# Performance work log

Measured on AMD Instinct MI355X. Metric: run time of the kernel, lower is better.

## Reference

```python
import jax, jax.numpy as jnp
import numpy as np

LAYER_SPECS = [(2, 4, 1), (2, 4, 1), (1, 4, 1), (1, 4, 1)]
SKIPS = [(k - s) * d for (s, k, d) in LAYER_SPECS]  # (ksz-stride)*dilation
C = 80  # encoder channels


def _conv1d(x, w, b, stride, dilation):
    # x: (N, Cin, L), w: (Cout, Cin, K)
    out = jax.lax.conv_general_dilated(
        x, w, window_strides=(stride,), padding='VALID',
        rhs_dilation=(dilation,), dimension_numbers=('NCH', 'OIH', 'NCH'))
    return out + b[None, :, None]


def _encoder(x, w_wide, b_wide, w_1x1, b_1x1, w_f0, b_f0, w_f1, b_f1):
    # x: (N, T, 80) -> (N, T', 80)
    x = jnp.transpose(x, (0, 2, 1))  # (N, 80, T)
    for i, ((stride, ksz, dil), skip) in enumerate(zip(LAYER_SPECS, SKIPS)):
        x1 = _conv1d(x, w_wide[i], b_wide[i], stride, dil)  # (N, 2C, L')
        a, g = jnp.split(x1, 2, axis=1)
        x2 = jnp.tanh(a) * jax.nn.sigmoid(g)                # gated activation
        x3 = _conv1d(x2, w_1x1[i], b_1x1[i], 1, 1)          # (N, C, L')
        if i == 0:
            x = x3
        else:
            T3 = x3.shape[2]
            # residual: strided slice of previous x, take last of each stride group
            res = x[:, :, skip:skip + T3 * stride].reshape(x.shape[0], C, T3, stride)[:, :, :, -1]
            x = x3 + res
    x = _conv1d(jax.nn.relu(_conv1d(x, w_f0, b_f0, 1, 1)), w_f1, b_f1, 1, 1)
    return jnp.transpose(x, (0, 2, 1))  # (N, T', 80)


def setup_inputs() -> dict:
    key = jax.random.key(0)
    ks = jax.random.split(key, 10)
    N, Ts, Tq = 16, 8192, 2048
    return {
        'search': jax.random.normal(ks[0], (N, Ts, 80), dtype=jnp.float32),
        'query': jax.random.normal(ks[1], (N, Tq, 80), dtype=jnp.float32),
        'w_wide': jax.random.normal(ks[2], (4, 160, 80, 4), dtype=jnp.float32) * 0.02,
        'b_wide': jnp.zeros((4, 160), dtype=jnp.float32),
        'w_1x1': jax.random.normal(ks[3], (4, 80, 80, 1), dtype=jnp.float32) * 0.05,
        'b_1x1': jnp.zeros((4, 80), dtype=jnp.float32),
        'w_f0': jax.random.normal(ks[4], (80, 80, 1), dtype=jnp.float32) * 0.05,
        'b_f0': jnp.zeros((80,), dtype=jnp.float32),
        'w_f1': jax.random.normal(ks[5], (80, 80, 1), dtype=jnp.float32) * 0.05,
        'b_f1': jax.random.normal(ks[6], (80,), dtype=jnp.float32) * 0.05,
        'embedding': jax.random.normal(ks[7], (1, 512, 80), dtype=jnp.float32) * 0.001,
        'w_lin': jax.random.normal(ks[8], (2, 80), dtype=jnp.float32) * 0.05,
        'b_lin': jnp.zeros((2,), dtype=jnp.float32),
    }


def reference(search, query, w_wide, b_wide, w_1x1, b_1x1,
              w_f0, b_f0, w_f1, b_f1, embedding, w_lin, b_lin):
    enc_s = _encoder(search, w_wide, b_wide, w_1x1, b_1x1, w_f0, b_f0, w_f1, b_f1)
    enc_q = _encoder(query, w_wide, b_wide, w_1x1, b_1x1, w_f0, b_f0, w_f1, b_f1)

    # ---- VectorQuant (no normalize): nearest-codeword lookup + straight-through ----
    x = enc_s[:, :, None, :]                  # (N, T, 1, V)
    N, T, nc, V = x.shape
    n_classes = embedding.shape[1]
    x1 = x.reshape(N * T, nc, V)              # (NT, 1, V)
    # squared-distance via expansion: argmin identical to argmin of L2 norm
    x2 = jnp.sum(x1 * x1, axis=-1, keepdims=True)          # (NT, 1, 1)
    e2 = jnp.sum(embedding * embedding, axis=-1)[None]     # (1, 1, K)
    xe = jnp.einsum('ncv,ckv->nck', x1, embedding)         # (NT, 1, K)
    idx = jnp.argmin(x2 - 2.0 * xe + e2, axis=2)           # (NT, 1)
    offset = jnp.arange(nc) * n_classes
    flat = embedding.reshape(-1, V)
    output = flat[(idx + offset[None, :]).reshape(-1)].reshape(x.shape)
    out0 = jax.lax.stop_gradient(output - x) + x           # straight-through
    discrete = out0[:, :, 0, :]               # (N, Ts', V)

    # ---- align query to search length, classify, max-pool over time ----
    sf = discrete.shape[1] // enc_q.shape[1]
    q = jnp.tile(enc_q, (1, sf, 1))
    pad = discrete.shape[1] - q.shape[1]
    q = jnp.pad(q, ((0, 0), (0, pad), (0, 0)))
    pred = jnp.tanh((q + discrete) @ w_lin.T + b_lin)      # (N, Ts', 2)
    return jnp.max(pred, axis=1)                           # (N, 2)
```

## Files before the change

kernel.cpp:

```cpp
#include <hip/hip_runtime.h>
#include <math.h>


#define NBATCH 16

typedef __attribute__((ext_vector_type(8))) short s16x8;
typedef __attribute__((ext_vector_type(4))) float f32x4;

__device__ __forceinline__ float fast_sigmoid(float x){ return 1.0f/(1.0f+__expf(-x)); }
__device__ __forceinline__ float fast_tanh(float x){ return 2.0f/(1.0f+__expf(-2.0f*x))-1.0f; }
__device__ __forceinline__ unsigned short f2bf(float f){
    unsigned int u = __float_as_uint(f);
    return (unsigned short)((u + 0x7FFFu + ((u >> 16) & 1u)) >> 16);
}
__device__ __forceinline__ unsigned int pk2bf(float lo, float hi){
    unsigned int r;
    asm("v_cvt_pk_bf16_f32 %0, %1, %2" : "=v"(r) : "v"(lo), "v"(hi));
    return r;
}
__device__ __forceinline__ unsigned short cvt1bf(float v){
    return (unsigned short)pk2bf(v, v);
}
__device__ __forceinline__ float bf2f(unsigned short s){
    return __uint_as_float(((unsigned int)s) << 16);
}

__global__ __launch_bounds__(256) void pack_all(
    const float* __restrict__ w_wide, const float* __restrict__ w_1x1,
    const float* __restrict__ wf0,    const float* __restrict__ wf1,
    const float* __restrict__ emb,
    unsigned short* __restrict__ WW, unsigned short* __restrict__ W1,
    unsigned short* __restrict__ F0, unsigned short* __restrict__ F1,
    unsigned short* __restrict__ EM, float* __restrict__ e2o)
{
    int i = blockIdx.x * 256 + threadIdx.x;
    if (i < 204800) {
        int l = i / 51200, r = i % 51200, oc = r / 320, k = r % 320;
        int j = k / 80, ic = k % 80;
        WW[i] = f2bf(w_wide[l * 51200 + oc * 320 + ic * 4 + j]);
    } else if (i < 235520) {
        int idx = i - 204800, l = idx / 7680, r = idx % 7680, oc = r / 96, k = r % 96;
        W1[idx] = (k < 80) ? f2bf(w_1x1[l * 6400 + oc * 80 + k]) : (unsigned short)0;
    } else if (i < 243200) {
        int idx = i - 235520, oc = idx / 96, k = idx % 96;
        F0[idx] = (k < 80) ? f2bf(wf0[oc * 80 + k]) : (unsigned short)0;
    } else if (i < 250880) {
        int idx = i - 243200, oc = idx / 96, k = idx % 96;
        F1[idx] = (k < 80) ? f2bf(wf1[oc * 80 + k]) : (unsigned short)0;
    } else if (i < 291840) {
        EM[i - 250880] = f2bf(emb[i - 250880]);
    } else if (i < 292352) {
        int e = i - 291840;
        float s = 0.f;
        for (int k = 0; k < 80; ++k) { float v = emb[e * 80 + k]; s = fmaf(v, v, s); }
        e2o[e] = s;
    }
}

template<int S, bool HAS_RES, bool FINAL>
__global__ __launch_bounds__(320, 3) void enc_layer(
    const float* __restrict__ xS, const float* __restrict__ xQ,
    const unsigned short* __restrict__ ww,  const float* __restrict__ wb,
    const unsigned short* __restrict__ w1p, const float* __restrict__ b1,
    float* __restrict__ outS, float* __restrict__ outQ,
    int TinS, int ToutS, int TinQ, int ToutQ, int nbS)
{
    constexpr int MT   = 4;
    constexpr int P    = 63 * S + 4;
    constexpr int HALF = (S == 2) ? 65 : 67;
    constexpr int NPARY= (S == 2) ? 2 : 1;
    constexpr int NEL  = P * 20;
    constexpr int NST  = (NEL + 319) / 320;

    __shared__ __attribute__((aligned(16))) unsigned short xs[NPARY * HALF * 88];
    __shared__ __attribute__((aligned(16))) unsigned short gsA[64 * 104];

    const int tid  = threadIdx.x;
    const int wave = tid >> 6;
    const int lane = tid & 63;
    const int m    = lane & 15;
    const int quad = lane >> 4;
    const int quad8 = quad * 8;
    const int c    = wave * 16 + m;
    const int n_   = blockIdx.y;

    const float* x; float* out; int T_in, T_out, bx;
    if ((int)blockIdx.x < nbS) { x = xS; out = outS; T_in = TinS; T_out = ToutS; bx = blockIdx.x; }
    else                       { x = xQ; out = outQ; T_in = TinQ; T_out = ToutQ; bx = blockIdx.x - nbS; }
    const int t0 = bx * 64;
    const long base_in = (long)n_ * T_in * 80;

    float4 vst[NST]; int odx[NST]; bool okw[NST];
#pragma unroll
    for (int it = 0; it < NST; ++it) {
        int u = tid + it * 320;
        okw[it] = (u < NEL);
        if (u >= NEL) u = NEL - 1;
        int pos = u / 20, c4 = u % 20;
        int tp = t0 * S + pos; if (tp > T_in - 1) tp = T_in - 1;
        vst[it] = *(const float4*)(x + base_in + (long)tp * 80 + c4 * 4);
        int row = (S == 2) ? (pos >> 1) : pos;
        int par = (S == 2) ? (pos & 1) : 0;
        odx[it] = (par * HALF + row) * 88 + c4 * 4;
    }

    const unsigned short* wa_base = ww + (long)c * 320 + quad8;
    const unsigned short* wg_base = ww + (long)(80 + c) * 320 + quad8;
    s16x8 baP[3], bgP[3];
    baP[0] = *(const s16x8*)(wa_base);       bgP[0] = *(const s16x8*)(wg_base);
    baP[1] = *(const s16x8*)(wa_base + 32);  bgP[1] = *(const s16x8*)(wg_base + 32);

    const unsigned short* wb1 = w1p + (long)c * 96 + quad8;
    s16x8 w1b0 = *(const s16x8*)(wb1);
    s16x8 w1b1 = *(const s16x8*)(wb1 + 32);
    s16x8 w1b2 = *(const s16x8*)(wb1 + 64);

#pragma unroll
    for (int it = 0; it < NST; ++it) {
        if (okw[it]) {
            float4 v = vst[it];
            *(uint2*)&xs[odx[it]] = make_uint2(pk2bf(v.x, v.y), pk2bf(v.z, v.w));
        }
    }

    f32x4 acc_a[MT], acc_g[MT];
#pragma unroll
    for (int mt = 0; mt < MT; ++mt) {
        acc_a[mt] = (f32x4){0.f, 0.f, 0.f, 0.f};
        acc_g[mt] = (f32x4){0.f, 0.f, 0.f, 0.f};
    }

    __syncthreads();

#pragma unroll
    for (int kk = 0; kk < 10; ++kk) {
        if (kk + 2 < 10) {
            baP[(kk + 2) % 3] = *(const s16x8*)(wa_base + (kk + 2) * 32);
            bgP[(kk + 2) % 3] = *(const s16x8*)(wg_base + (kk + 2) * 32);
        }
        const int kq = kk * 32 + quad8;
        const int j  = (kq >= 240) ? 3 : ((kq >= 160) ? 2 : ((kq >= 80) ? 1 : 0));
        const int ic0 = kq - j * 80;
        int xb;
        if (S == 2) xb = ((j & 1) * HALF + (j >> 1)) * 88 + ic0;
        else        xb = j * 88 + ic0;
        s16x8 a[MT];
#pragma unroll
        for (int mt = 0; mt < MT; ++mt)
            a[mt] = *(const s16x8*)&xs[xb + (mt * 16 + m) * 88];
        s16x8 ba = baP[kk % 3], bg = bgP[kk % 3];
#pragma unroll
        for (int mt = 0; mt < MT; ++mt) {
            acc_a[mt] = __builtin_amdgcn_mfma_f32_16x16x32_bf16(a[mt], ba, acc_a[mt], 0, 0, 0);
            acc_g[mt] = __builtin_amdgcn_mfma_f32_16x16x32_bf16(a[mt], bg, acc_g[mt], 0, 0, 0);
        }
    }

    const float ba_b = wb[c];
    const float bg_b = wb[80 + c];
#pragma unroll
    for (int mt = 0; mt < MT; ++mt)
#pragma unroll
        for (int r = 0; r < 4; ++r) {
            float av = acc_a[mt][r] + ba_b;
            float gv = acc_g[mt][r] + bg_b;
            gsA[(mt * 16 + quad * 4 + r) * 104 + c] =
                cvt1bf(fast_tanh(av) * fast_sigmoid(gv));
        }
    const uint4 z4 = make_uint4(0u, 0u, 0u, 0u);
    for (int u = tid; u < 128; u += 320)
        *(uint4*)&gsA[(u >> 1) * 104 + 80 + (u & 1) * 8] = z4;
    __syncthreads();

    f32x4 a1[MT];
#pragma unroll
    for (int mt = 0; mt < MT; ++mt) a1[mt] = (f32x4){0.f, 0.f, 0.f, 0.f};
#pragma unroll
    for (int kb = 0; kb < 3; ++kb) {
        s16x8 b = (kb == 0) ? w1b0 : ((kb == 1) ? w1b1 : w1b2);
#pragma unroll
        for (int mt = 0; mt < MT; ++mt) {
            s16x8 ag = *(const s16x8*)&gsA[(mt * 16 + m) * 104 + kb * 32 + quad8];
            a1[mt] = __builtin_amdgcn_mfma_f32_16x16x32_bf16(ag, b, a1[mt], 0, 0, 0);
        }
    }

    const long base_out = (long)n_ * T_out * 80;
    const float b1c = b1[c];
#pragma unroll
    for (int mt = 0; mt < MT; ++mt)
#pragma unroll
        for (int r = 0; r < 4; ++r) {
            int tg = t0 + mt * 16 + quad * 4 + r;
            if (tg < T_out)
                out[base_out + (long)tg * 80 + c] = a1[mt][r] + b1c;
        }
}

__global__ __launch_bounds__(320, 2) void enc_fuse123(
    const float* __restrict__ xS, const float* __restrict__ xQ,
    const unsigned short* __restrict__ WW, const float* __restrict__ WB,
    const unsigned short* __restrict__ W1, const float* __restrict__ BB1,
    const unsigned short* __restrict__ F0p, const float* __restrict__ BF0,
    const unsigned short* __restrict__ F1p, const float* __restrict__ BF1,
    float* __restrict__ outS, float* __restrict__ outQ,
    int TinS, int ToutS, int TinQ, int ToutQ, int nbS)
{
    constexpr int AOFF = 0, B1OFF = 12496, B2OFF = 19776, GOFF = 26744;
    constexpr int NEL = 142 * 20, NST = 9;
    __shared__ __attribute__((aligned(16))) unsigned short Ld[35064];

    const int tid  = threadIdx.x;
    const int wave = tid >> 6;
    const int lane = tid & 63;
    const int m    = lane & 15;
    const int quad = lane >> 4;
    const int quad8 = quad * 8;
    const int c    = wave * 16 + m;
    const int n_   = blockIdx.y;

    const float* x; float* out; int TinA, Tout, bx;
    if ((int)blockIdx.x < nbS) { x = xS; out = outS; TinA = TinS; Tout = ToutS; bx = blockIdx.x; }
    else                       { x = xQ; out = outQ; TinA = TinQ; Tout = ToutQ; bx = blockIdx.x - nbS; }
    const int t0 = bx * 64;
    const long base_in = (long)n_ * TinA * 80;
    const long base_out = (long)n_ * Tout * 80;

    float4 vst[NST]; int odx[NST]; bool okw[NST];
#pragma unroll
    for (int it = 0; it < NST; ++it) {
        int u = tid + it * 320;
        okw[it] = (u < NEL);
        if (u >= NEL) u = NEL - 1;
        int pos = u / 20, c4 = u % 20;
        int ra = 2 * t0 + pos; if (ra > TinA - 1) ra = TinA - 1;
        vst[it] = *(const float4*)(x + base_in + (long)ra * 80 + c4 * 4);
        odx[it] = ((pos & 1) * 71 + (pos >> 1)) * 88 + c4 * 4;
    }

    const unsigned short* wa1 = WW + 51200 + (long)c * 320 + quad8;
    const unsigned short* wg1 = WW + 51200 + (long)(80 + c) * 320 + quad8;
    s16x8 baP[3], bgP[3];
    baP[0] = *(const s16x8*)(wa1);       bgP[0] = *(const s16x8*)(wg1);
    baP[1] = *(const s16x8*)(wa1 + 32);  bgP[1] = *(const s16x8*)(wg1 + 32);
    const unsigned short* w1l1 = W1 + 7680 + (long)c * 96 + quad8;
    s16x8 wA0 = *(const s16x8*)(w1l1);
    s16x8 wA1 = *(const s16x8*)(w1l1 + 32);
    s16x8 wA2 = *(const s16x8*)(w1l1 + 64);

#pragma unroll
    for (int it = 0; it < NST; ++it) {
        if (okw[it]) {
            float4 v = vst[it];
            *(uint2*)&Ld[AOFF + odx[it]] = make_uint2(pk2bf(v.x, v.y), pk2bf(v.z, v.w));
        }
    }
    const uint4 z4 = make_uint4(0u, 0u, 0u, 0u);
    for (int u = tid; u < 160; u += 320)
        *(uint4*)&Ld[GOFF + (u >> 1) * 104 + 80 + (u & 1) * 8] = z4;

    f32x4 aa[5], ag[5];
#pragma unroll
    for (int mt = 0; mt < 5; ++mt) {
        aa[mt] = (f32x4){0.f, 0.f, 0.f, 0.f};
        ag[mt] = (f32x4){0.f, 0.f, 0.f, 0.f};
    }
    __syncthreads();

    auto mm96 = [&](s16x8 b0, s16x8 b1f, s16x8 b2, int goff, f32x4 (&o)[5]) {
#pragma unroll
        for (int mt = 0; mt < 5; ++mt) o[mt] = (f32x4){0.f, 0.f, 0.f, 0.f};
#pragma unroll
        for (int kb = 0; kb < 3; ++kb) {
            s16x8 b = (kb == 0) ? b0 : ((kb == 1) ? b1f : b2);
#pragma unroll
            for (int mt = 0; mt < 5; ++mt) {
                s16x8 agf = *(const s16x8*)&Ld[goff + (mt * 16 + m) * 104 + kb * 32 + quad8];
                o[mt] = __builtin_amdgcn_mfma_f32_16x16x32_bf16(agf, b, o[mt], 0, 0, 0);
            }
        }
    };

#pragma unroll
    for (int kk = 0; kk < 10; ++kk) {
        if (kk + 2 < 10) {
            baP[(kk + 2) % 3] = *(const s16x8*)(wa1 + (kk + 2) * 32);
            bgP[(kk + 2) % 3] = *(const s16x8*)(wg1 + (kk + 2) * 32);
        }
        const int kq = kk * 32 + quad8;
        const int j  = (kq >= 240) ? 3 : ((kq >= 160) ? 2 : ((kq >= 80) ? 1 : 0));
        const int ic0 = kq - j * 80;
        const int xb = (j & 1) * 6248 + (j >> 1) * 88 + ic0;
        s16x8 a[5];
#pragma unroll
        for (int mt = 0; mt < 5; ++mt)
            a[mt] = *(const s16x8*)&Ld[AOFF + xb + (mt * 16 + m) * 88];
        s16x8 ba = baP[kk % 3], bg = bgP[kk % 3];
#pragma unroll
        for (int mt = 0; mt < 5; ++mt) {
            aa[mt] = __builtin_amdgcn_mfma_f32_16x16x32_bf16(a[mt], ba, aa[mt], 0, 0, 0);
            ag[mt] = __builtin_amdgcn_mfma_f32_16x16x32_bf16(a[mt], bg, ag[mt], 0, 0, 0);
        }
    }
    {
        const float bab = WB[160 + c], bgb = WB[160 + 80 + c];
#pragma unroll
        for (int mt = 0; mt < 5; ++mt)
#pragma unroll
            for (int r = 0; r < 4; ++r) {
                int row = mt * 16 + quad * 4 + r;
                float av = aa[mt][r] + bab, gv = ag[mt][r] + bgb;
                Ld[GOFF + row * 104 + c] = cvt1bf(fast_tanh(av) * fast_sigmoid(gv));
            }
    }
    __syncthreads();
    {
        f32x4 o[5];
        mm96(wA0, wA1, wA2, GOFF, o);
        const float b1c = BB1[80 + c];
#pragma unroll
        for (int mt = 0; mt < 5; ++mt)
#pragma unroll
            for (int r = 0; r < 4; ++r) {
                int row = mt * 16 + quad * 4 + r;
                if (row < 70) {
                    float res = bf2f(Ld[AOFF + 6248 + (row + 1) * 88 + c]);
                    Ld[B1OFF + row * 104 + c] = cvt1bf(o[mt][r] + b1c + res);
                }
            }
    }
    const unsigned short* wa2 = WW + 102400 + (long)c * 320 + quad8;
    const unsigned short* wg2 = WW + 102400 + (long)(80 + c) * 320 + quad8;
    baP[0] = *(const s16x8*)(wa2);       bgP[0] = *(const s16x8*)(wg2);
    baP[1] = *(const s16x8*)(wa2 + 32);  bgP[1] = *(const s16x8*)(wg2 + 32);
    const unsigned short* w1l2 = W1 + 15360 + (long)c * 96 + quad8;
    wA0 = *(const s16x8*)(w1l2);
    wA1 = *(const s16x8*)(w1l2 + 32);
    wA2 = *(const s16x8*)(w1l2 + 64);
    __syncthreads();

#pragma unroll
    for (int mt = 0; mt < 5; ++mt) {
        aa[mt] = (f32x4){0.f, 0.f, 0.f, 0.f};
        ag[mt] = (f32x4){0.f, 0.f, 0.f, 0.f};
    }
#pragma unroll
    for (int kk = 0; kk < 10; ++kk) {
        if (kk + 2 < 10) {
            baP[(kk + 2) % 3] = *(const s16x8*)(wa2 + (kk + 2) * 32);
            bgP[(kk + 2) % 3] = *(const s16x8*)(wg2 + (kk + 2) * 32);
        }
        const int kq = kk * 32 + quad8;
        const int j  = (kq >= 240) ? 3 : ((kq >= 160) ? 2 : ((kq >= 80) ? 1 : 0));
        const int ic0 = kq - j * 80;
        const int xb = j * 104 + ic0;
        s16x8 a[5];
#pragma unroll
        for (int mt = 0; mt < 5; ++mt)
            a[mt] = *(const s16x8*)&Ld[B1OFF + xb + (mt * 16 + m) * 104];
        s16x8 ba = baP[kk % 3], bg = bgP[kk % 3];
#pragma unroll
        for (int mt = 0; mt < 5; ++mt) {
            aa[mt] = __builtin_amdgcn_mfma_f32_16x16x32_bf16(a[mt], ba, aa[mt], 0, 0, 0);
            ag[mt] = __builtin_amdgcn_mfma_f32_16x16x32_bf16(a[mt], bg, ag[mt], 0, 0, 0);
        }
    }
    {
        const float bab = WB[320 + c], bgb = WB[320 + 80 + c];
#pragma unroll
        for (int mt = 0; mt < 5; ++mt)
#pragma unroll
            for (int r = 0; r < 4; ++r) {
                int row = mt * 16 + quad * 4 + r;
                float av = aa[mt][r] + bab, gv = ag[mt][r] + bgb;
                Ld[GOFF + row * 104 + c] = cvt1bf(fast_tanh(av) * fast_sigmoid(gv));
            }
    }
    __syncthreads();
    {
        f32x4 o[5];
        mm96(wA0, wA1, wA2, GOFF, o);
        const float b1c = BB1[160 + c];
#pragma unroll
        for (int mt = 0; mt < 5; ++mt)
#pragma unroll
            for (int r = 0; r < 4; ++r) {
                int row = mt * 16 + quad * 4 + r;
                if (row < 67) {
                    float res = bf2f(Ld[B1OFF + (row + 3) * 104 + c]);
                    Ld[B2OFF + row * 104 + c] = cvt1bf(o[mt][r] + b1c + res);
                }
            }
    }
    const unsigned short* wa3 = WW + 153600 + (long)c * 320 + quad8;
    const unsigned short* wg3 = WW + 153600 + (long)(80 + c) * 320 + quad8;
    baP[0] = *(const s16x8*)(wa3);       bgP[0] = *(const s16x8*)(wg3);
    baP[1] = *(const s16x8*)(wa3 + 32);  bgP[1] = *(const s16x8*)(wg3 + 32);
    const unsigned short* w1l3 = W1 + 23040 + (long)c * 96 + quad8;
    wA0 = *(const s16x8*)(w1l3);
    wA1 = *(const s16x8*)(w1l3 + 32);
    wA2 = *(const s16x8*)(w1l3 + 64);
    __syncthreads();

#pragma unroll
    for (int mt = 0; mt < 5; ++mt) {
        aa[mt] = (f32x4){0.f, 0.f, 0.f, 0.f};
        ag[mt] = (f32x4){0.f, 0.f, 0.f, 0.f};
    }
#pragma unroll
    for (int kk = 0; kk < 10; ++kk) {
        if (kk + 2 < 10) {
            baP[(kk + 2) % 3] = *(const s16x8*)(wa3 + (kk + 2) * 32);
            bgP[(kk + 2) % 3] = *(const s16x8*)(wg3 + (kk + 2) * 32);
        }
        const int kq = kk * 32 + quad8;
        const int j  = (kq >= 240) ? 3 : ((kq >= 160) ? 2 : ((kq >= 80) ? 1 : 0));
        const int ic0 = kq - j * 80;
        const int xb = j * 104 + ic0;
        s16x8 a[5];
#pragma unroll
        for (int mt = 0; mt < 5; ++mt)
            a[mt] = *(const s16x8*)&Ld[B2OFF + xb + (mt * 16 + m) * 104];
        s16x8 ba = baP[kk % 3], bg = bgP[kk % 3];
#pragma unroll
        for (int mt = 0; mt < 5; ++mt) {
            aa[mt] = __builtin_amdgcn_mfma_f32_16x16x32_bf16(a[mt], ba, aa[mt], 0, 0, 0);
            ag[mt] = __builtin_amdgcn_mfma_f32_16x16x32_bf16(a[mt], bg, ag[mt], 0, 0, 0);
        }
    }
    {
        const float bab = WB[480 + c], bgb = WB[480 + 80 + c];
#pragma unroll
        for (int mt = 0; mt < 5; ++mt)
#pragma unroll
            for (int r = 0; r < 4; ++r) {
                int row = mt * 16 + quad * 4 + r;
                float av = aa[mt][r] + bab, gv = ag[mt][r] + bgb;
                Ld[GOFF + row * 104 + c] = cvt1bf(fast_tanh(av) * fast_sigmoid(gv));
            }
    }
    for (int u = tid; u < 160; u += 320)
        *(uint4*)&Ld[AOFF + (u >> 1) * 104 + 80 + (u & 1) * 8] = z4;
    __syncthreads();
    {
        f32x4 o[5];
        mm96(wA0, wA1, wA2, GOFF, o);
        const float b1c = BB1[240 + c];
#pragma unroll
        for (int mt = 0; mt < 5; ++mt)
#pragma unroll
            for (int r = 0; r < 4; ++r) {
                int row = mt * 16 + quad * 4 + r;
                float res = bf2f(Ld[B2OFF + (row + 3) * 104 + c]);
                Ld[AOFF + row * 104 + c] = cvt1bf(o[mt][r] + b1c + res);
            }
    }
    const unsigned short* wf0b = F0p + (long)c * 96 + quad8;
    s16x8 f0b0 = *(const s16x8*)(wf0b);
    s16x8 f0b1 = *(const s16x8*)(wf0b + 32);
    s16x8 f0b2 = *(const s16x8*)(wf0b + 64);
    __syncthreads();
    {
        f32x4 o[5];
        mm96(f0b0, f0b1, f0b2, AOFF, o);
        const float bf0c = BF0[c];
#pragma unroll
        for (int mt = 0; mt < 5; ++mt)
#pragma unroll
            for (int r = 0; r < 4; ++r) {
                int row = mt * 16 + quad * 4 + r;
                Ld[GOFF + row * 104 + c] = cvt1bf(fmaxf(o[mt][r] + bf0c, 0.f));
            }
    }
    const unsigned short* wf1b = F1p + (long)c * 96 + quad8;
    s16x8 f1b0 = *(const s16x8*)(wf1b);
    s16x8 f1b1 = *(const s16x8*)(wf1b + 32);
    s16x8 f1b2 = *(const s16x8*)(wf1b + 64);
    __syncthreads();
    {
        f32x4 o[5];
        mm96(f1b0, f1b1, f1b2, GOFF, o);
        const float bf1c = BF1[c];
#pragma unroll
        for (int mt = 0; mt < 4; ++mt)
#pragma unroll
            for (int r = 0; r < 4; ++r) {
                int tg = t0 + mt * 16 + quad * 4 + r;
                if (tg < Tout)
                    out[base_out + (long)tg * 80 + c] = o[mt][r] + bf1c;
            }
    }
}

__global__ __launch_bounds__(256, 2) void vq_mfma(
    const float* __restrict__ enc_s, const float* __restrict__ enc_q,
    const unsigned short* __restrict__ embp, const float* __restrict__ emb,
    const float* __restrict__ e2v,
    const float* __restrict__ w_lin, const float* __restrict__ b_lin,
    float* __restrict__ pred)
{
    __shared__ unsigned short xs[64 * 104];
    __shared__ unsigned short es[128 * 104];
    const uint4 z4 = make_uint4(0u, 0u, 0u, 0u);

    const int tid  = threadIdx.x;
    const int wave = tid >> 6;
    const int lane = tid & 63;
    const int m    = lane & 15;
    const int quad = lane >> 4;
    const int n    = blockIdx.y;
    const int t0   = blockIdx.x * 64;

    for (int u = tid; u < 64 * 20; u += 256) {
        int row = u / 20, c4 = u % 20;
        int t = t0 + row; if (t > 2039) t = 2039;
        float4 v = *(const float4*)(enc_s + ((long)n * 2040 + t) * 80 + c4 * 4);
        unsigned int s0 = (unsigned int)f2bf(v.x) | ((unsigned int)f2bf(v.y) << 16);
        unsigned int s1 = (unsigned int)f2bf(v.z) | ((unsigned int)f2bf(v.w) << 16);
        *(uint2*)&xs[row * 104 + c4 * 4] = make_uint2(s0, s1);
    }
    for (int u = tid; u < 128; u += 256)
        *(uint4*)&xs[(u >> 1) * 104 + 80 + (u & 1) * 8] = z4;
    __syncthreads();

    s16x8 af[3];
#pragma unroll
    for (int kb = 0; kb < 3; ++kb)
        af[kb] = *(const s16x8*)&xs[(wave * 16 + m) * 104 + kb * 32 + quad * 8];

    float best[4]; int bi[4];
#pragma unroll
    for (int r = 0; r < 4; ++r) { best[r] = 1e30f; bi[r] = 0; }

    for (int ch = 0; ch < 4; ++ch) {
        const int c0 = ch * 128;
        __syncthreads();
        for (int u = tid; u < 128 * 12; u += 256) {
            int el = u / 12, seg = u % 12;
            uint4 v = z4;
            if (seg < 10) v = *(const uint4*)(embp + (long)(c0 + el) * 80 + seg * 8);
            *(uint4*)&es[el * 104 + seg * 8] = v;
        }
        __syncthreads();

        f32x4 acc[8];
#pragma unroll
        for (int nt = 0; nt < 8; ++nt) acc[nt] = (f32x4){0.f, 0.f, 0.f, 0.f};
#pragma unroll
        for (int kb = 0; kb < 3; ++kb) {
            const int k0 = kb * 32 + quad * 8;
#pragma unroll
            for (int nt = 0; nt < 8; ++nt) {
                s16x8 b = *(const s16x8*)&es[(nt * 16 + m) * 104 + k0];
                acc[nt] = __builtin_amdgcn_mfma_f32_16x16x32_bf16(af[kb], b, acc[nt], 0, 0, 0);
            }
        }
#pragma unroll
        for (int nt = 0; nt < 8; ++nt) {
            const int e = c0 + nt * 16 + m;
            const float e2x = e2v[e];
#pragma unroll
            for (int r = 0; r < 4; ++r) {
                float s = fmaf(-2.0f, acc[nt][r], e2x);
                if (s < best[r]) { best[r] = s; bi[r] = e; }
            }
        }
    }

    __syncthreads();
    float* rb = (float*)es;
    int*   ri = (int*)es + 1088;
#pragma unroll
    for (int r = 0; r < 4; ++r) {
        int tl = wave * 16 + quad * 4 + r;
        rb[tl * 17 + m] = best[r];
        ri[tl * 17 + m] = bi[r];
    }
    __syncthreads();

    if (tid < 64) {
        const int t = t0 + tid;
        float b = rb[tid * 17]; int ix = ri[tid * 17];
#pragma unroll
        for (int j = 1; j < 16; ++j) {
            float v = rb[tid * 17 + j]; int iv = ri[tid * 17 + j];
            if (v < b || (v == b && iv < ix)) { b = v; ix = iv; }
        }
        if (t < 2040) {
            const float4* ev = (const float4*)(emb + (long)ix * 80);
            const bool hasq = (t < 2016);
            const float4* qv = hasq
                ? (const float4*)(enc_q + ((long)n * 504 + (t % 504)) * 80) : nullptr;
            float p0 = b_lin[0], p1 = b_lin[1];
#pragma unroll
            for (int i = 0; i < 20; ++i) {
                float4 e4 = ev[i];
                float4 q4 = hasq ? qv[i] : make_float4(0.f, 0.f, 0.f, 0.f);
                float4 w0 = *(const float4*)(w_lin + 4 * i);
                float4 w1 = *(const float4*)(w_lin + 80 + 4 * i);
                float sx = e4.x + q4.x, sy = e4.y + q4.y;
                float sz = e4.z + q4.z, sw = e4.w + q4.w;
                p0 = fmaf(sx, w0.x, p0); p1 = fmaf(sx, w1.x, p1);
                p0 = fmaf(sy, w0.y, p0); p1 = fmaf(sy, w1.y, p1);
                p0 = fmaf(sz, w0.z, p0); p1 = fmaf(sz, w1.z, p1);
                p0 = fmaf(sw, w0.w, p0); p1 = fmaf(sw, w1.w, p1);
            }
            long o = ((long)n * 2040 + t) * 2;
            pred[o]     = fast_tanh(p0);
            pred[o + 1] = fast_tanh(p1);
        }
    }
}

__global__ __launch_bounds__(256) void max_red(const float* __restrict__ pred,
                                               float* __restrict__ out)
{
    __shared__ float s0[256], s1[256];
    const int n = blockIdx.x, tid = threadIdx.x;
    float m0 = -1e30f, m1 = -1e30f;
    for (int t = tid; t < 2040; t += 256) {
        long o = ((long)n * 2040 + t) * 2;
        m0 = fmaxf(m0, pred[o]);
        m1 = fmaxf(m1, pred[o + 1]);
    }
    s0[tid] = m0; s1[tid] = m1;
    __syncthreads();
    for (int st = 128; st > 0; st >>= 1) {
        if (tid < st) {
            s0[tid] = fmaxf(s0[tid], s0[tid + st]);
            s1[tid] = fmaxf(s1[tid], s1[tid + st]);
        }
        __syncthreads();
    }
    if (tid == 0) { out[n * 2] = s0[0]; out[n * 2 + 1] = s1[0]; }
}

extern "C" void kernel_launch(void* const* d_in, const int* in_sizes, int n_in,
                              void* d_out, int out_size, void* d_ws, size_t ws_size,
                              hipStream_t stream)
{
    const float* search = (const float*)d_in[0];
    const float* query  = (const float*)d_in[1];
    const float* w_wide = (const float*)d_in[2];
    const float* b_wide = (const float*)d_in[3];
    const float* w_1x1  = (const float*)d_in[4];
    const float* b_1x1  = (const float*)d_in[5];
    const float* w_f0   = (const float*)d_in[6];
    const float* b_f0   = (const float*)d_in[7];
    const float* w_f1   = (const float*)d_in[8];
    const float* b_f1   = (const float*)d_in[9];
    const float* emb    = (const float*)d_in[10];
    const float* w_lin  = (const float*)d_in[11];
    const float* b_lin  = (const float*)d_in[12];
    float* out = (float*)d_out;
    float* ws  = (float*)d_ws;

    float* A  = ws;
    float* B  = A  + 5241600;
    float* C  = B  + 2618880;
    float* QA = C  + 2618880;
    float* QB = QA + 1309440;
    float* QC = QB + 652800;
    unsigned short* WWp = (unsigned short*)(QC + 652800);
    unsigned short* W1p = WWp + 204800;
    unsigned short* F0p = W1p + 30720;
    unsigned short* F1p = F0p + 7680;
    unsigned short* EMp = F1p + 7680;
    float* e2b = (float*)(EMp + 40960);

    const dim3 blk(320);
    auto nb = [](int T) { return (T + 63) / 64; };

    pack_all<<<dim3(1142), dim3(256), 0, stream>>>(w_wide, w_1x1, w_f0, w_f1, emb,
                                                   WWp, W1p, F0p, F1p, EMp, e2b);

    enc_layer<2, false, false><<<dim3(nb(4095) + nb(1023), NBATCH), blk, 0, stream>>>(
        search, query, WWp, b_wide, W1p, b_1x1,
        A, QA, 8192, 4095, 2048, 1023, nb(4095));

    enc_fuse123<<<dim3(nb(2040) + nb(504), NBATCH), blk, 0, stream>>>(
        A, QA, WWp, b_wide, W1p, b_1x1, F0p, b_f0, F1p, b_f1,
        B, QB, 4095, 2040, 1023, 504, nb(2040));

    vq_mfma<<<dim3(32, NBATCH), dim3(256), 0, stream>>>(B, QB, EMp, emb, e2b,
                                                        w_lin, b_lin, C);
    max_red<<<dim3(NBATCH), dim3(256), 0, stream>>>(C, out);
}
```

Baseline: 242.4 us.

## Halve fused encoder tile to 32 outputs for smaller LDS and higher occupancy

Cuts the fused layers-1..3 encoder tile from 64 to 32 output timesteps per block. The LDS buffers shrink accordingly and several strides tighten from 104 to 88, and the launch bound is raised to allow 5 blocks per CU. The goal is more resident waves and more blocks to balance across CUs. The cost is a larger share of halo recomputation, since each block now recomputes about 78 input rows to produce 32 outputs, along with more padded MFMA work per useful row.

```diff
diff --git a/kernel.cpp b/kernel.cpp
--- a/kernel.cpp
+++ b/kernel.cpp
@@ -197,7 +197,7 @@
         }
 }
 
-__global__ __launch_bounds__(320, 2) void enc_fuse123(
+__global__ __launch_bounds__(320, 5) void enc_fuse123(
     const float* __restrict__ xS, const float* __restrict__ xQ,
     const unsigned short* __restrict__ WW, const float* __restrict__ WB,
     const unsigned short* __restrict__ W1, const float* __restrict__ BB1,
@@ -206,9 +206,10 @@
     float* __restrict__ outS, float* __restrict__ outQ,
     int TinS, int ToutS, int TinQ, int ToutQ, int nbS)
 {
-    constexpr int AOFF = 0, B1OFF = 12496, B2OFF = 19776, GOFF = 26744;
-    constexpr int NEL = 142 * 20, NST = 9;
-    __shared__ __attribute__((aligned(16))) unsigned short Ld[35064];
+    constexpr int AOFF = 0, APAR = 3432;
+    constexpr int B1OFF = 6864, B2OFF = 10208, GOFF = 13288;
+    constexpr int NEL = 78 * 20, NST = 5;
+    __shared__ __attribute__((aligned(16))) unsigned short Ld[18280];
 
     const int tid  = threadIdx.x;
     const int wave = tid >> 6;
@@ -222,7 +223,7 @@
     const float* x; float* out; int TinA, Tout, bx;
     if ((int)blockIdx.x < nbS) { x = xS; out = outS; TinA = TinS; Tout = ToutS; bx = blockIdx.x; }
     else                       { x = xQ; out = outQ; TinA = TinQ; Tout = ToutQ; bx = blockIdx.x - nbS; }
-    const int t0 = bx * 64;
+    const int t0 = bx * 32;
     const long base_in = (long)n_ * TinA * 80;
     const long base_out = (long)n_ * Tout * 80;
 
@@ -235,7 +236,7 @@
         int pos = u / 20, c4 = u % 20;
         int ra = 2 * t0 + pos; if (ra > TinA - 1) ra = TinA - 1;
         vst[it] = *(const float4*)(x + base_in + (long)ra * 80 + c4 * 4);
-        odx[it] = ((pos & 1) * 71 + (pos >> 1)) * 88 + c4 * 4;
+        odx[it] = ((pos & 1) * 39 + (pos >> 1)) * 88 + c4 * 4;
     }
 
     const unsigned short* wa1 = WW + 51200 + (long)c * 320 + quad8;
@@ -256,25 +257,38 @@
         }
     }
     const uint4 z4 = make_uint4(0u, 0u, 0u, 0u);
-    for (int u = tid; u < 160; u += 320)
+    for (int u = tid; u < 96; u += 320)
         *(uint4*)&Ld[GOFF + (u >> 1) * 104 + 80 + (u & 1) * 8] = z4;
 
-    f32x4 aa[5], ag[5];
-#pragma unroll
-    for (int mt = 0; mt < 5; ++mt) {
+    f32x4 aa[3], ag[3];
+#pragma unroll
+    for (int mt = 0; mt < 3; ++mt) {
         aa[mt] = (f32x4){0.f, 0.f, 0.f, 0.f};
         ag[mt] = (f32x4){0.f, 0.f, 0.f, 0.f};
     }
     __syncthreads();
 
-    auto mm96 = [&](s16x8 b0, s16x8 b1f, s16x8 b2, int goff, f32x4 (&o)[5]) {
-#pragma unroll
-        for (int mt = 0; mt < 5; ++mt) o[mt] = (f32x4){0.f, 0.f, 0.f, 0.f};
+    auto mm96_3 = [&](s16x8 b0, s16x8 b1f, s16x8 b2, int goff, f32x4 (&o)[3]) {
+#pragma unroll
+        for (int mt = 0; mt < 3; ++mt) o[mt] = (f32x4){0.f, 0.f, 0.f, 0.f};
 #pragma unroll
         for (int kb = 0; kb < 3; ++kb) {
             s16x8 b = (kb == 0) ? b0 : ((kb == 1) ? b1f : b2);
 #pragma unroll
-            for (int mt = 0; mt < 5; ++mt) {
+            for (int mt = 0; mt < 3; ++mt) {
+                s16x8 agf = *(const s16x8*)&Ld[goff + (mt * 16 + m) * 104 + kb * 32 + quad8];
+                o[mt] = __builtin_amdgcn_mfma_f32_16x16x32_bf16(agf, b, o[mt], 0, 0, 0);
+            }
+        }
+    };
+    auto mm96_2 = [&](s16x8 b0, s16x8 b1f, s16x8 b2, int goff, f32x4 (&o)[2]) {
+#pragma unroll
+        for (int mt = 0; mt < 2; ++mt) o[mt] = (f32x4){0.f, 0.f, 0.f, 0.f};
+#pragma unroll
+        for (int kb = 0; kb < 3; ++kb) {
+            s16x8 b = (kb == 0) ? b0 : ((kb == 1) ? b1f : b2);
+#pragma unroll
+            for (int mt = 0; mt < 2; ++mt) {
                 s16x8 agf = *(const s16x8*)&Ld[goff + (mt * 16 + m) * 104 + kb * 32 + quad8];
                 o[mt] = __builtin_amdgcn_mfma_f32_16x16x32_bf16(agf, b, o[mt], 0, 0, 0);
             }
@@ -290,14 +304,14 @@
         const int kq = kk * 32 + quad8;
         const int j  = (kq >= 240) ? 3 : ((kq >= 160) ? 2 : ((kq >= 80) ? 1 : 0));
         const int ic0 = kq - j * 80;
-        const int xb = (j & 1) * 6248 + (j >> 1) * 88 + ic0;
-        s16x8 a[5];
-#pragma unroll
-        for (int mt = 0; mt < 5; ++mt)
+        const int xb = (j & 1) * APAR + (j >> 1) * 88 + ic0;
+        s16x8 a[3];
+#pragma unroll
+        for (int mt = 0; mt < 3; ++mt)
             a[mt] = *(const s16x8*)&Ld[AOFF + xb + (mt * 16 + m) * 88];
         s16x8 ba = baP[kk % 3], bg = bgP[kk % 3];
 #pragma unroll
-        for (int mt = 0; mt < 5; ++mt) {
+        for (int mt = 0; mt < 3; ++mt) {
             aa[mt] = __builtin_amdgcn_mfma_f32_16x16x32_bf16(a[mt], ba, aa[mt], 0, 0, 0);
             ag[mt] = __builtin_amdgcn_mfma_f32_16x16x32_bf16(a[mt], bg, ag[mt], 0, 0, 0);
         }
@@ -305,7 +319,7 @@
     {
         const float bab = WB[160 + c], bgb = WB[160 + 80 + c];
 #pragma unroll
-        for (int mt = 0; mt < 5; ++mt)
+        for (int mt = 0; mt < 3; ++mt)
 #pragma unroll
             for (int r = 0; r < 4; ++r) {
                 int row = mt * 16 + quad * 4 + r;
@@ -315,17 +329,17 @@
     }
     __syncthreads();
     {
-        f32x4 o[5];
-        mm96(wA0, wA1, wA2, GOFF, o);
+        f32x4 o[3];
+        mm96_3(wA0, wA1, wA2, GOFF, o);
         const float b1c = BB1[80 + c];
 #pragma unroll
-        for (int mt = 0; mt < 5; ++mt)
+        for (int mt = 0; mt < 3; ++mt)
 #pragma unroll
             for (int r = 0; r < 4; ++r) {
                 int row = mt * 16 + quad * 4 + r;
-                if (row < 70) {
-                    float res = bf2f(Ld[AOFF + 6248 + (row + 1) * 88 + c]);
-                    Ld[B1OFF + row * 104 + c] = cvt1bf(o[mt][r] + b1c + res);
+                if (row < 38) {
+                    float res = bf2f(Ld[AOFF + APAR + (row + 1) * 88 + c]);
+                    Ld[B1OFF + row * 88 + c] = cvt1bf(o[mt][r] + b1c + res);
                 }
             }
     }
@@ -340,11 +354,6 @@
     __syncthreads();
 
 #pragma unroll
-    for (int mt = 0; mt < 5; ++mt) {
-        aa[mt] = (f32x4){0.f, 0.f, 0.f, 0.f};
-        ag[mt] = (f32x4){0.f, 0.f, 0.f, 0.f};
-    }
-#pragma unroll
     for (int kk = 0; kk < 10; ++kk) {
         if (kk + 2 < 10) {
             baP[(kk + 2) % 3] = *(const s16x8*)(wa2 + (kk + 2) * 32);
@@ -353,14 +362,21 @@
         const int kq = kk * 32 + quad8;
         const int j  = (kq >= 240) ? 3 : ((kq >= 160) ? 2 : ((kq >= 80) ? 1 : 0));
         const int ic0 = kq - j * 80;
-        const int xb = j * 104 + ic0;
-        s16x8 a[5];
-#pragma unroll
-        for (int mt = 0; mt < 5; ++mt)
-            a[mt] = *(const s16x8*)&Ld[B1OFF + xb + (mt * 16 + m) * 104];
+        const int xb = j * 88 + ic0;
+        s16x8 a[3];
+#pragma unroll
+        for (int mt = 0; mt < 3; ++mt)
+            a[mt] = *(const s16x8*)&Ld[B1OFF + xb + (mt * 16 + m) * 88];
         s16x8 ba = baP[kk % 3], bg = bgP[kk % 3];
-#pragma unroll
-        for (int mt = 0; mt < 5; ++mt) {
+        if (kk == 0) {
+#pragma unroll
+            for (int mt = 0; mt < 3; ++mt) {
+                aa[mt] = (f32x4){0.f, 0.f, 0.f, 0.f};
+                ag[mt] = (f32x4){0.f, 0.f, 0.f, 0.f};
+            }
+        }
+#pragma unroll
+        for (int mt = 0; mt < 3; ++mt) {
             aa[mt] = __builtin_amdgcn_mfma_f32_16x16x32_bf16(a[mt], ba, aa[mt], 0, 0, 0);
             ag[mt] = __builtin_amdgcn_mfma_f32_16x16x32_bf16(a[mt], bg, ag[mt], 0, 0, 0);
         }
@@ -368,7 +384,7 @@
     {
         const float bab = WB[320 + c], bgb = WB[320 + 80 + c];
 #pragma unroll
-        for (int mt = 0; mt < 5; ++mt)
+        for (int mt = 0; mt < 3; ++mt)
 #pragma unroll
             for (int r = 0; r < 4; ++r) {
                 int row = mt * 16 + quad * 4 + r;
@@ -378,17 +394,17 @@
     }
     __syncthreads();
     {
-        f32x4 o[5];
-        mm96(wA0, wA1, wA2, GOFF, o);
+        f32x4 o[3];
+        mm96_3(wA0, wA1, wA2, GOFF, o);
         const float b1c = BB1[160 + c];
 #pragma unroll
-        for (int mt = 0; mt < 5; ++mt)
+        for (int mt = 0; mt < 3; ++mt)
 #pragma unroll
             for (int r = 0; r < 4; ++r) {
                 int row = mt * 16 + quad * 4 + r;
-                if (row < 67) {
-                    float res = bf2f(Ld[B1OFF + (row + 3) * 104 + c]);
-                    Ld[B2OFF + row * 104 + c] = cvt1bf(o[mt][r] + b1c + res);
+                if (row < 35) {
+                    float res = bf2f(Ld[B1OFF + (row + 3) * 88 + c]);
+                    Ld[B2OFF + row * 88 + c] = cvt1bf(o[mt][r] + b1c + res);
                 }
             }
     }
@@ -403,11 +419,6 @@
     __syncthreads();
 
 #pragma unroll
-    for (int mt = 0; mt < 5; ++mt) {
-        aa[mt] = (f32x4){0.f, 0.f, 0.f, 0.f};
-        ag[mt] = (f32x4){0.f, 0.f, 0.f, 0.f};
-    }
-#pragma unroll
     for (int kk = 0; kk < 10; ++kk) {
         if (kk + 2 < 10) {
             baP[(kk + 2) % 3] = *(const s16x8*)(wa3 + (kk + 2) * 32);
@@ -416,14 +427,21 @@
         const int kq = kk * 32 + quad8;
         const int j  = (kq >= 240) ? 3 : ((kq >= 160) ? 2 : ((kq >= 80) ? 1 : 0));
         const int ic0 = kq - j * 80;
-        const int xb = j * 104 + ic0;
-        s16x8 a[5];
-#pragma unroll
-        for (int mt = 0; mt < 5; ++mt)
-            a[mt] = *(const s16x8*)&Ld[B2OFF + xb + (mt * 16 + m) * 104];
+        const int xb = j * 88 + ic0;
+        s16x8 a[3];
+#pragma unroll
+        for (int mt = 0; mt < 3; ++mt)
+            a[mt] = *(const s16x8*)&Ld[B2OFF + xb + (mt * 16 + m) * 88];
         s16x8 ba = baP[kk % 3], bg = bgP[kk % 3];
-#pragma unroll
-        for (int mt = 0; mt < 5; ++mt) {
+        if (kk == 0) {
+#pragma unroll
+            for (int mt = 0; mt < 3; ++mt) {
+                aa[mt] = (f32x4){0.f, 0.f, 0.f, 0.f};
+                ag[mt] = (f32x4){0.f, 0.f, 0.f, 0.f};
+            }
+        }
+#pragma unroll
+        for (int mt = 0; mt < 3; ++mt) {
             aa[mt] = __builtin_amdgcn_mfma_f32_16x16x32_bf16(a[mt], ba, aa[mt], 0, 0, 0);
             ag[mt] = __builtin_amdgcn_mfma_f32_16x16x32_bf16(a[mt], bg, ag[mt], 0, 0, 0);
         }
@@ -431,7 +449,7 @@
     {
         const float bab = WB[480 + c], bgb = WB[480 + 80 + c];
 #pragma unroll
-        for (int mt = 0; mt < 5; ++mt)
+        for (int mt = 0; mt < 3; ++mt)
 #pragma unroll
             for (int r = 0; r < 4; ++r) {
                 int row = mt * 16 + quad * 4 + r;
@@ -439,19 +457,19 @@
                 Ld[GOFF + row * 104 + c] = cvt1bf(fast_tanh(av) * fast_sigmoid(gv));
             }
     }
-    for (int u = tid; u < 160; u += 320)
+    for (int u = tid; u < 64; u += 320)
         *(uint4*)&Ld[AOFF + (u >> 1) * 104 + 80 + (u & 1) * 8] = z4;
     __syncthreads();
     {
-        f32x4 o[5];
-        mm96(wA0, wA1, wA2, GOFF, o);
+        f32x4 o[2];
+        mm96_2(wA0, wA1, wA2, GOFF, o);
         const float b1c = BB1[240 + c];
 #pragma unroll
-        for (int mt = 0; mt < 5; ++mt)
+        for (int mt = 0; mt < 2; ++mt)
 #pragma unroll
             for (int r = 0; r < 4; ++r) {
                 int row = mt * 16 + quad * 4 + r;
-                float res = bf2f(Ld[B2OFF + (row + 3) * 104 + c]);
+                float res = bf2f(Ld[B2OFF + (row + 3) * 88 + c]);
                 Ld[AOFF + row * 104 + c] = cvt1bf(o[mt][r] + b1c + res);
             }
     }
@@ -461,11 +479,11 @@
     s16x8 f0b2 = *(const s16x8*)(wf0b + 64);
     __syncthreads();
     {
-        f32x4 o[5];
-        mm96(f0b0, f0b1, f0b2, AOFF, o);
+        f32x4 o[2];
+        mm96_2(f0b0, f0b1, f0b2, AOFF, o);
         const float bf0c = BF0[c];
 #pragma unroll
-        for (int mt = 0; mt < 5; ++mt)
+        for (int mt = 0; mt < 2; ++mt)
 #pragma unroll
             for (int r = 0; r < 4; ++r) {
                 int row = mt * 16 + quad * 4 + r;
@@ -478,11 +496,11 @@
     s16x8 f1b2 = *(const s16x8*)(wf1b + 64);
     __syncthreads();
     {
-        f32x4 o[5];
-        mm96(f1b0, f1b1, f1b2, GOFF, o);
+        f32x4 o[2];
+        mm96_2(f1b0, f1b1, f1b2, GOFF, o);
         const float bf1c = BF1[c];
 #pragma unroll
-        for (int mt = 0; mt < 4; ++mt)
+        for (int mt = 0; mt < 2; ++mt)
 #pragma unroll
             for (int r = 0; r < 4; ++r) {
                 int tg = t0 + mt * 16 + quad * 4 + r;
@@ -669,18 +687,19 @@
     float* e2b = (float*)(EMp + 40960);
 
     const dim3 blk(320);
-    auto nb = [](int T) { return (T + 63) / 64; };
+    auto nb64 = [](int T) { return (T + 63) / 64; };
+    auto nb32 = [](int T) { return (T + 31) / 32; };
 
     pack_all<<<dim3(1142), dim3(256), 0, stream>>>(w_wide, w_1x1, w_f0, w_f1, emb,
                                                    WWp, W1p, F0p, F1p, EMp, e2b);
 
-    enc_layer<2, false, false><<<dim3(nb(4095) + nb(1023), NBATCH), blk, 0, stream>>>(
+    enc_layer<2, false, false><<<dim3(nb64(4095) + nb64(1023), NBATCH), blk, 0, stream>>>(
         search, query, WWp, b_wide, W1p, b_1x1,
-        A, QA, 8192, 4095, 2048, 1023, nb(4095));
-
-    enc_fuse123<<<dim3(nb(2040) + nb(504), NBATCH), blk, 0, stream>>>(
+        A, QA, 8192, 4095, 2048, 1023, nb64(4095));
+
+    enc_fuse123<<<dim3(nb32(2040) + nb32(504), NBATCH), blk, 0, stream>>>(
         A, QA, WWp, b_wide, W1p, b_1x1, F0p, b_f0, F1p, b_f1,
-        B, QB, 4095, 2040, 1023, 504, nb(2040));
+        B, QB, 4095, 2040, 1023, 504, nb32(2040));
 
     vq_mfma<<<dim3(32, NBATCH), dim3(256), 0, stream>>>(B, QB, EMp, emb, e2b,
                                                         w_lin, b_lin, C);
```

Result: faster. 236.8 us (-2.3%).
